# Optimization experiments

Hardware: AMD Instinct MI355X
Metric: run time of the kernel (lower is better)

Reference implementation:

```python
import jax, jax.numpy as jnp
import numpy as np

B, N, H, D = 4, 16384, 8, 128
KERNEL_SIZE, STRIDE = 32, 16


def setup_inputs() -> dict:
    key = jax.random.key(0)
    k1, k2, k3 = jax.random.split(key, 3)
    x = jax.random.normal(k1, (B, N, H, D), dtype=jnp.float32)
    weight = jax.random.normal(k2, (KERNEL_SIZE,), dtype=jnp.float32)
    pe = jax.random.normal(k3, (KERNEL_SIZE, D), dtype=jnp.float32)
    return {"x": x, "weight": weight, "pe": pe}


def reference(x, weight, pe):
    # y[b,m,h,d] = sum_k (x[b, m*stride + k, h, d] + pe[k,d]) * w[k] / kernel_size
    Bx, Nx, Hx, Dx = x.shape
    K = weight.shape[0]
    M = (Nx - K) // STRIDE + 1  # num_blocks
    # window gather indices [M, K]
    idx = jnp.arange(M)[:, None] * STRIDE + jnp.arange(K)[None, :]
    xw = x[:, idx]  # [B, M, K, H, D]
    # split the pe term out: sum_k pe[k]*w[k] is a constant [D] vector
    y = jnp.einsum('bmkhd,k->bmhd', xw, weight) + jnp.einsum('kd,k->d', pe, weight)
    return (y / K).astype(x.dtype)
```

## Files before the change

### kernel.cpp

```cpp
#include <hip/hip_runtime.h>

#define Bc 4
#define Nc 16384
#define Hc 8
#define Dc 128
#define Kc 32
#define STRIDEc 16
#define Mc 1023

__global__ __launch_bounds__(256) void compress_kv_kernel(
    const float* __restrict__ x,
    const float* __restrict__ w,
    const float* __restrict__ pe,
    float* __restrict__ out)
{
    __shared__ float s_w[Kc];
    __shared__ __align__(16) float s_bias[Dc];

    const int tid = threadIdx.x;

    if (tid < Kc) s_w[tid] = w[tid] * (1.0f / (float)Kc);
    __syncthreads();

    if (tid < Dc) {
        float b = 0.0f;
        #pragma unroll 8
        for (int k = 0; k < Kc; ++k) b += pe[k * Dc + tid] * s_w[k];
        s_bias[tid] = b;
    }
    __syncthreads();

    const int bm = blockIdx.x;
    const int m  = bm % Mc;
    const int b  = bm / Mc;
    const int d4 = tid & 31;
    const int h  = tid >> 5;

    const float4* __restrict__ x4 = (const float4*)x;

    int base = ((b * Nc + m * STRIDEc) * Hc + h) * (Dc / 4) + d4;
    const int step = Hc * (Dc / 4);

    float4 acc = ((const float4*)s_bias)[d4];

    #pragma unroll 8
    for (int k = 0; k < Kc; ++k) {
        float4 xv = x4[base + k * step];
        float wk = s_w[k];
        acc.x += xv.x * wk;
        acc.y += xv.y * wk;
        acc.z += xv.z * wk;
        acc.w += xv.w * wk;
    }

    float4* __restrict__ out4 = (float4*)out;
    const int obase = ((b * Mc + m) * Hc + h) * (Dc / 4) + d4;
    out4[obase] = acc;
}

extern "C" void kernel_launch(void* const* d_in, const int* in_sizes, int n_in,
                              void* d_out, int out_size, void* d_ws, size_t ws_size,
                              hipStream_t stream) {
    const float* x  = (const float*)d_in[0];
    const float* w  = (const float*)d_in[1];
    const float* pe = (const float*)d_in[2];
    float* out = (float*)d_out;

    const int grid = Bc * Mc;
    compress_kv_kernel<<<grid, 256, 0, stream>>>(x, w, pe, out);
}
```

Baseline: 371.8 us.

## Compute two overlapping windows per block sharing half-window partial sums

```diff
diff --git a/kernel.cpp b/kernel.cpp
--- a/kernel.cpp
+++ b/kernel.cpp
@@ -7,55 +7,98 @@
 #define Kc 32
 #define STRIDEc 16
 #define Mc 1023
+#define HD4 (Hc * Dc / 4)
+#define WPB 2
+#define BLKS_PER_B 512
+#define GRIDc (Bc * BLKS_PER_B)
 
-__global__ __launch_bounds__(256) void compress_kv_kernel(
+__global__ __launch_bounds__(256, 4) void compress_kv_kernel(
     const float* __restrict__ x,
     const float* __restrict__ w,
     const float* __restrict__ pe,
     float* __restrict__ out)
 {
-    __shared__ float s_w[Kc];
-    __shared__ __align__(16) float s_bias[Dc];
+    const int bid = blockIdx.x;
+    const int swz = (bid & 7) * (GRIDc / 8) + (bid >> 3);
+
+    const int b  = swz >> 9;
+    const int m0 = (swz & (BLKS_PER_B - 1)) * WPB;
+    const bool two = (m0 + 1 < Mc);
 
     const int tid = threadIdx.x;
+    const int d4  = tid & 31;
+    const int h   = tid >> 5;
 
-    if (tid < Kc) s_w[tid] = w[tid] * (1.0f / (float)Kc);
-    __syncthreads();
+    float wr[Kc];
+    #pragma unroll
+    for (int k = 0; k < Kc; ++k) wr[k] = w[k];
 
-    if (tid < Dc) {
-        float b = 0.0f;
-        #pragma unroll 8
-        for (int k = 0; k < Kc; ++k) b += pe[k * Dc + tid] * s_w[k];
-        s_bias[tid] = b;
+    const float4* __restrict__ pe4 = (const float4*)pe;
+    float4 bias = make_float4(0.f, 0.f, 0.f, 0.f);
+    #pragma unroll
+    for (int k = 0; k < Kc; ++k) {
+        float4 p = pe4[k * (Dc / 4) + d4];
+        float a = wr[k];
+        bias.x += p.x * a; bias.y += p.y * a;
+        bias.z += p.z * a; bias.w += p.w * a;
     }
-    __syncthreads();
-
-    const int bm = blockIdx.x;
-    const int m  = bm % Mc;
-    const int b  = bm / Mc;
-    const int d4 = tid & 31;
-    const int h  = tid >> 5;
 
     const float4* __restrict__ x4 = (const float4*)x;
+    int base = ((b * Nc + m0 * STRIDEc) * Hc + h) * (Dc / 4) + d4;
 
-    int base = ((b * Nc + m * STRIDEc) * Hc + h) * (Dc / 4) + d4;
-    const int step = Hc * (Dc / 4);
+    float4 s0p, s0, s1;
 
-    float4 acc = ((const float4*)s_bias)[d4];
+    s0 = make_float4(0.f, 0.f, 0.f, 0.f);
+    #pragma unroll
+    for (int i = 0; i < 16; ++i) {
+        float4 xv = x4[base + i * HD4];
+        float a = wr[i];
+        s0.x += xv.x * a; s0.y += xv.y * a;
+        s0.z += xv.z * a; s0.w += xv.w * a;
+    }
+    s0p = s0;
+    base += 16 * HD4;
 
-    #pragma unroll 8
-    for (int k = 0; k < Kc; ++k) {
-        float4 xv = x4[base + k * step];
-        float wk = s_w[k];
-        acc.x += xv.x * wk;
-        acc.y += xv.y * wk;
-        acc.z += xv.z * wk;
-        acc.w += xv.w * wk;
+    s0 = make_float4(0.f, 0.f, 0.f, 0.f);
+    s1 = make_float4(0.f, 0.f, 0.f, 0.f);
+    #pragma unroll
+    for (int i = 0; i < 16; ++i) {
+        float4 xv = x4[base + i * HD4];
+        float a = wr[i], c = wr[16 + i];
+        s0.x += xv.x * a; s0.y += xv.y * a;
+        s0.z += xv.z * a; s0.w += xv.w * a;
+        s1.x += xv.x * c; s1.y += xv.y * c;
+        s1.z += xv.z * c; s1.w += xv.w * c;
     }
 
     float4* __restrict__ out4 = (float4*)out;
-    const int obase = ((b * Mc + m) * Hc + h) * (Dc / 4) + d4;
-    out4[obase] = acc;
+    int obase = ((b * Mc + m0) * Hc + h) * (Dc / 4) + d4;
+    const float inv = 1.0f / (float)Kc;
+
+    float4 r;
+    r.x = (s0p.x + s1.x + bias.x) * inv;
+    r.y = (s0p.y + s1.y + bias.y) * inv;
+    r.z = (s0p.z + s1.z + bias.z) * inv;
+    r.w = (s0p.w + s1.w + bias.w) * inv;
+    out4[obase] = r;
+
+    if (two) {
+        s0p = s0;
+        base += 16 * HD4;
+        s1 = make_float4(0.f, 0.f, 0.f, 0.f);
+        #pragma unroll
+        for (int i = 0; i < 16; ++i) {
+            float4 xv = x4[base + i * HD4];
+            float c = wr[16 + i];
+            s1.x += xv.x * c; s1.y += xv.y * c;
+            s1.z += xv.z * c; s1.w += xv.w * c;
+        }
+        r.x = (s0p.x + s1.x + bias.x) * inv;
+        r.y = (s0p.y + s1.y + bias.y) * inv;
+        r.z = (s0p.z + s1.z + bias.z) * inv;
+        r.w = (s0p.w + s1.w + bias.w) * inv;
+        out4[obase + HD4] = r;
+    }
 }
 
 extern "C" void kernel_launch(void* const* d_in, const int* in_sizes, int n_in,
@@ -66,6 +109,5 @@
     const float* pe = (const float*)d_in[2];
     float* out = (float*)d_out;
 
-    const int grid = Bc * Mc;
-    compress_kv_kernel<<<grid, 256, 0, stream>>>(x, w, pe, out);
+    compress_kv_kernel<<<GRIDc, 256, 0, stream>>>(x, w, pe, out);
 }
```

New measurement: 363.7 us. 2.2% less time.
